# Optimization experiments

Measured on AMD Instinct MI355X. Metric: run time of the kernel, lower is better.

Reference implementation:

```python
import jax, jax.numpy as jnp
import numpy as np

EMBED_DIM = 768
N_HEADS = 12
SEQ_LEN = 577
MAX_REL = 2


def _relative_position_indices(seq_len: int, max_rel: int) -> jnp.ndarray:
    """Static [S, S] int index map into the relative bias table."""
    n_patches = seq_len - 1
    n_per_dim = int(np.sqrt(n_patches))
    n_entries = (2 * max_rel - 1) ** 2
    cls_cls, cls_patch, patch_cls = n_entries, n_entries + 1, n_entries + 2
    idx = np.arange(seq_len)
    qy, qx = (idx - 1) // n_per_dim, (idx - 1) % n_per_dim
    ry = np.clip(qy[:, None] - qy[None, :], -max_rel + 1, max_rel - 1)
    rx = np.clip(qx[:, None] - qx[None, :], -max_rel + 1, max_rel - 1)
    patch_idx = (ry + max_rel - 1) * (2 * max_rel - 1) + (rx + max_rel - 1)
    is_cls = idx == 0
    out = np.where(is_cls[None, :], patch_cls, patch_idx)
    out = np.where(is_cls[:, None], cls_patch, out)
    out = np.where(is_cls[:, None] & is_cls[None, :], cls_cls, out)
    return jnp.asarray(out, dtype=jnp.int32)


def setup_inputs() -> dict:
    key = jax.random.key(0)
    ks = jax.random.split(key, 6)
    e = EMBED_DIM
    scale = 1.0 / np.sqrt(e)
    return {
        "x": jax.random.normal(ks[0], (32, SEQ_LEN, e), dtype=jnp.float32),
        "Wq": jax.random.normal(ks[1], (e, e), dtype=jnp.float32) * scale,
        "Wk": jax.random.normal(ks[2], (e, e), dtype=jnp.float32) * scale,
        "Wv": jax.random.normal(ks[3], (e, e), dtype=jnp.float32) * scale,
        "Wo": jax.random.normal(ks[4], (e, e), dtype=jnp.float32) * scale,
        "bo": jnp.zeros((e,), dtype=jnp.float32),
        "bias_table": jax.random.normal(ks[5], (12,), dtype=jnp.float32) * 0.02,
    }


def reference(x, Wq, Wk, Wv, Wo, bo, bias_table):
    b, s, e = x.shape
    h, d = N_HEADS, e // N_HEADS
    rel_idx = _relative_position_indices(s, MAX_REL)  # [S, S] int32 (static)

    q = (x @ Wq).reshape(b, s, h, d).transpose(0, 2, 1, 3)  # [b,h,s,d]
    k = (x @ Wk).reshape(b, s, h, d).transpose(0, 2, 1, 3)
    v = (x @ Wv).reshape(b, s, h, d).transpose(0, 2, 1, 3)

    scores = jnp.einsum('bhqd,bhkd->bhqk', q, k) / jnp.sqrt(jnp.float32(d))
    bias = jnp.take(bias_table, rel_idx, axis=0)  # [S, S]
    attn = jax.nn.softmax(scores + bias[None, None, :, :], axis=-1)

    out = jnp.einsum('bhqk,bhkd->bhqd', attn, v)
    out = out.transpose(0, 2, 1, 3).reshape(b, s, e)
    return out @ Wo + bo
```

## Files before the change

kernel.cpp:

```cpp
#include <hip/hip_runtime.h>

typedef unsigned short u16;
typedef short short8 __attribute__((ext_vector_type(8)));
typedef float floatx4 __attribute__((ext_vector_type(4)));

#define MFMA16(a, b, c) __builtin_amdgcn_mfma_f32_16x16x32_bf16((a), (b), (c), 0, 0, 0)

__device__ __forceinline__ u16 f2bf(float f) {
  unsigned u = __builtin_bit_cast(unsigned, f);
  u = (u + 0x7fffu + ((u >> 16) & 1u)) >> 16;
  return (u16)u;
}

__device__ __forceinline__ float exp2hw(float x) {
  float r; asm("v_exp_f32 %0, %1" : "=v"(r) : "v"(x)); return r;
}

__device__ __forceinline__ unsigned cvtpk_bf16(float lo, float hi) {
  unsigned r;
  asm("v_cvt_pk_bf16_f32 %0, %1, %2" : "=v"(r) : "v"(lo), "v"(hi));
  return r;
}

__device__ __forceinline__ float bflo(unsigned u) {
  return __builtin_bit_cast(float, u << 16);
}
__device__ __forceinline__ float bfhi(unsigned u) {
  return __builtin_bit_cast(float, u & 0xffff0000u);
}

__device__ __forceinline__ void gload16(const void* g, void* l) {
  typedef __attribute__((address_space(1))) const void GV;
  typedef __attribute__((address_space(3))) void LV;
  __builtin_amdgcn_global_load_lds((GV*)g, (LV*)l, 16, 0, 0);
}


__global__ void cvt_x_kernel(const float* __restrict__ x, u16* __restrict__ xb, int n4) {
  int i = blockIdx.x * 256 + threadIdx.x;
  if (i >= n4) return;
  float4 v = ((const float4*)x)[i];
  ushort4 r; r.x = f2bf(v.x); r.y = f2bf(v.y); r.z = f2bf(v.z); r.w = f2bf(v.w);
  ((ushort4*)xb)[i] = r;
}

__global__ void cvt_wT_kernel(const float* __restrict__ in, u16* __restrict__ out) {
  __shared__ float tile[64][65];
  const int k0 = blockIdx.x * 64, n0 = blockIdx.y * 64;
  const int t = threadIdx.x;
  const int tr = t >> 6, tc = t & 63;
#pragma unroll
  for (int i = 0; i < 16; ++i) {
    int row = i * 4 + tr;
    tile[row][tc] = in[(size_t)(k0 + row) * 768 + n0 + tc];
  }
  __syncthreads();
#pragma unroll
  for (int i = 0; i < 16; ++i) {
    int row = i * 4 + tr;
    out[(size_t)(n0 + row) * 768 + k0 + tc] = f2bf(tile[tc][row]);
  }
}

__global__ void bias_kernel(const float* __restrict__ table, u16* __restrict__ bp) {
  int idx = blockIdx.x * 256 + threadIdx.x;
  if (idx >= 577 * 76) return;
  int q = idx / 76, kb = idx - q * 76;
  u16 o8[8];
#pragma unroll
  for (int j = 0; j < 8; ++j) {
    int k = kb * 8 + j;
    float v = 0.f;
    if (k <= 576) {
      int id;
      if (q == 0 && k == 0) id = 9;
      else if (q == 0) id = 10;
      else if (k == 0) id = 11;
      else {
        int qy = (q - 1) / 24, qx = (q - 1) % 24;
        int ky = (k - 1) / 24, kx = (k - 1) % 24;
        int ry = qy - ky; ry = ry < -1 ? -1 : (ry > 1 ? 1 : ry);
        int rx = qx - kx; rx = rx < -1 ? -1 : (rx > 1 ? 1 : rx);
        id = (ry + 1) * 3 + (rx + 1);
      }
      v = table[id] * 1.4426950408889634f;
    }
    o8[j] = f2bf(v);
  }
  *(uint4*)(bp + ((size_t)kb * 577 + q) * 8) = *(const uint4*)o8;
}

__global__ void zero_vpad(u16* __restrict__ vT) {
  int i = blockIdx.x * 256 + threadIdx.x;
  if (i >= 384 * 64 * 31) return;
  int row = i / 31, c = i - (i / 31) * 31;
  vT[(size_t)row * 608 + 577 + c] = 0;
}


template <int MODE>
__global__ __launch_bounds__(256) void gemm_kernel(
    const u16* __restrict__ A, const u16* __restrict__ BT,
    const int M, const int NBN,
    float* __restrict__ outF, const float* __restrict__ bvec,
    u16* __restrict__ qarr, u16* __restrict__ karr, u16* __restrict__ vTa) {
  constexpr int K = 768;
  __shared__ __align__(16) u16 smem[17408];
  u16* As = smem;
  u16* Bs = smem + 8192;
  u16* Cs = smem;

  const int bid = blockIdx.x;
  const int nb = bid % NBN, mb = bid / NBN;
  const int tid = threadIdx.x;
  const int w = tid >> 6, l = tid & 63;
  const int wr = w >> 1, wc = w & 1;
  const int l15 = l & 15, l4 = l >> 4;
  const int m0 = mb * 128, n0 = nb * 128;

  floatx4 acc[4][4];
#pragma unroll
  for (int i = 0; i < 4; ++i)
#pragma unroll
    for (int j = 0; j < 4; ++j) acc[i][j] = 0.f;

  const int trow = tid >> 2;
  const int tk = (tid & 3) * 8;

  auto stage = [&](int buf, int kt) {
    const int k0 = kt * 32;
#pragma unroll
    for (int i = 0; i < 2; ++i) {
      int row = i * 64 + trow;
      int ar = m0 + row; if (ar >= M) ar = M - 1;
      gload16(A + (size_t)ar * K + k0 + tk, &As[buf * 4096 + row * 32 + tk]);
      int br = n0 + row;
      gload16(BT + (size_t)br * K + k0 + tk, &Bs[buf * 4096 + row * 32 + tk]);
    }
  };

  stage(0, 0);
  __syncthreads();
  int cur = 0;
  for (int kt = 0; kt < 24; ++kt) {
    if (kt + 1 < 24) stage(cur ^ 1, kt + 1);
    short8 af[4], bf[4];
#pragma unroll
    for (int mi = 0; mi < 4; ++mi)
      af[mi] = *(const short8*)&As[cur * 4096 + (wr * 64 + mi * 16 + l15) * 32 + l4 * 8];
#pragma unroll
    for (int ni = 0; ni < 4; ++ni)
      bf[ni] = *(const short8*)&Bs[cur * 4096 + (wc * 64 + ni * 16 + l15) * 32 + l4 * 8];
#pragma unroll
    for (int mi = 0; mi < 4; ++mi)
#pragma unroll
      for (int ni = 0; ni < 4; ++ni)
        acc[mi][ni] = MFMA16(af[mi], bf[ni], acc[mi][ni]);
    __syncthreads();
    cur ^= 1;
  }

  if constexpr (MODE == 0) {
    const int proj = nb / 6;
    const int h0 = (nb - proj * 6) * 2;
    const float qs = (proj == 0) ? 0.18033688011112042f : 1.0f;
#pragma unroll
    for (int mi = 0; mi < 4; ++mi)
#pragma unroll
      for (int i = 0; i < 4; ++i) {
        const int rloc = wr * 64 + mi * 16 + l4 * 4 + i;
#pragma unroll
        for (int ni = 0; ni < 4; ++ni) {
          const int cloc = wc * 64 + ni * 16 + l15;
          Cs[rloc * 136 + cloc] = f2bf(acc[mi][ni][i] * qs);
        }
      }
    __syncthreads();

    if (proj < 2) {
      u16* dst = (proj == 0) ? qarr : karr;
      const int r = tid >> 1, half = tid & 1;
      const int mrow = m0 + r;
      if (mrow < M) {
        const int bq = mrow / 577, sq = mrow - bq * 577;
        u16* base = dst + ((size_t)(bq * 12 + h0 + half) * 577 + sq) * 64;
        const u16* src = Cs + r * 136 + half * 64;
#pragma unroll
        for (int j = 0; j < 8; ++j)
          *(uint4*)(base + j * 8) = *(const uint4*)(src + j * 8);
      }
    } else {
      const int rr = tid & 127, chalf = tid >> 7;
      const int mrow = m0 + rr;
      if (mrow < M) {
        const int bq = mrow / 577, sq = mrow - bq * 577;
        u16* vbase = vTa + ((size_t)(bq * 12 + h0 + chalf) * 64) * 608 + sq;
        const u16* src = Cs + rr * 136 + chalf * 64;
#pragma unroll
        for (int dc = 0; dc < 8; ++dc) {
          const short8 vv = *(const short8*)(src + dc * 8);
#pragma unroll
          for (int jj = 0; jj < 8; ++jj)
            vbase[(size_t)(dc * 8 + jj) * 608] = (u16)vv[jj];
        }
      }
    }
  } else {
#pragma unroll
    for (int mi = 0; mi < 4; ++mi) {
#pragma unroll
      for (int i = 0; i < 4; ++i) {
        const int mrow = m0 + wr * 64 + mi * 16 + l4 * 4 + i;
        if (mrow >= M) continue;
#pragma unroll
        for (int ni = 0; ni < 4; ++ni) {
          const int ncol = n0 + wc * 64 + ni * 16 + l15;
          outF[(size_t)mrow * 768 + ncol] = acc[mi][ni][i] + bvec[ncol];
        }
      }
    }
  }
}


__global__ __launch_bounds__(256, 3) void attn_kernel(
    const u16* __restrict__ qg, const u16* __restrict__ kg,
    const u16* __restrict__ vT, const u16* __restrict__ bp,
    u16* __restrict__ xa) {
  const int bid = (blockIdx.x & 7) * 240 + (blockIdx.x >> 3);
  const int bh = bid / 5, qblk = bid - bh * 5;
  const int tid = threadIdx.x;
  const int w = tid >> 6, l = tid & 63;
  const int l15 = l & 15, l4 = l >> 4;
  const int qbase = qblk * 128 + w * 32;

  const u16* qh = qg + (size_t)bh * 577 * 64;
  const u16* kh = kg + (size_t)bh * 577 * 64;
  const u16* vh = vT + (size_t)bh * 64 * 608;

  __shared__ u16 Ks[2][32 * 64];
  __shared__ u16 Vs[2][32 * 64];

  const int e_ = l >> 3;
  const int s_ = l & 7;
  const int Rk = w * 8 + e_;
  const int kbK = s_ ^ ((4 * w + (e_ & 3)) & 7);
  const int dpV = w * 8 + e_;
  const int dV = 2 * dpV + (s_ >> 2);
  const int kvV = ((s_ & 3) ^ (e_ & 3)) * 8;

  const int sig = ((l15 >> 2) << 3) + (l15 & 3);
  const int sg = l15 & 7;
  const int offA0 = sig * 64 + ((l4 ^ sg)) * 8;
  const int offA1 = sig * 64 + (((l4 | 4) ^ sg)) * 8;
  const int offA2 = offA0 + 256;
  const int offA3 = offA1 + 256;
  const int dpr = l15 >> 1;
  const int offV = dpr * 64 + (((l15 & 1) << 2) + (l4 ^ (dpr & 3))) * 8;

  short8 qf[2][2];
  int bq[2];
#pragma unroll
  for (int g = 0; g < 2; ++g) {
    int qr = qbase + g * 16 + l15; if (qr > 576) qr = 576;
    bq[g] = qr;
    qf[g][0] = *(const short8*)(qh + qr * 64 + l4 * 8);
    qf[g][1] = *(const short8*)(qh + qr * 64 + 32 + l4 * 8);
  }

  floatx4 o[2][4];
  float m[2] = {-1e30f, -1e30f}, lsum[2] = {0.f, 0.f};
#pragma unroll
  for (int g = 0; g < 2; ++g)
#pragma unroll
    for (int d = 0; d < 4; ++d) o[g][d] = 0.f;

  {
    int kr = Rk; if (kr > 576) kr = 576;
    gload16(kh + (size_t)kr * 64 + kbK * 8, &Ks[0][w * 512 + l * 8]);
    gload16(vh + (size_t)dV * 608 + kvV, &Vs[0][w * 512 + l * 8]);
  }
  uint4 bc0 = *(const uint4*)(bp + ((size_t)l4 * 577 + bq[0]) * 8);
  uint4 bc1 = *(const uint4*)(bp + ((size_t)l4 * 577 + bq[1]) * 8);
  __syncthreads();

  for (int t = 0; t < 19; ++t) {
    const int cur = t & 1;
    const int kvb = t * 32;

    uint4 nb0 = bc0, nb1 = bc1;
    if (t < 18) {
      const int nkvb = kvb + 32;
      int kr = nkvb + Rk; if (kr > 576) kr = 576;
      gload16(kh + (size_t)kr * 64 + kbK * 8, &Ks[cur ^ 1][w * 512 + l * 8]);
      gload16(vh + (size_t)dV * 608 + nkvb + kvV, &Vs[cur ^ 1][w * 512 + l * 8]);
      const int nkb = (t + 1) * 4 + l4;
      nb0 = *(const uint4*)(bp + ((size_t)nkb * 577 + bq[0]) * 8);
      nb1 = *(const uint4*)(bp + ((size_t)nkb * 577 + bq[1]) * 8);
    }

    const u16* kb_ = &Ks[cur][0];
    const short8 A0 = *(const short8*)(kb_ + offA0);
    const short8 A1 = *(const short8*)(kb_ + offA1);
    const short8 A2 = *(const short8*)(kb_ + offA2);
    const short8 A3 = *(const short8*)(kb_ + offA3);
    const u16* vb_ = &Vs[cur][0];
    const short8 vf0 = *(const short8*)(vb_ + offV);
    const short8 vf1 = *(const short8*)(vb_ + offV + 512);
    const short8 vf2 = *(const short8*)(vb_ + offV + 1024);
    const short8 vf3 = *(const short8*)(vb_ + offV + 1536);

    float v0[8], v1[8];
    {
      floatx4 s0 = 0.f, s1 = 0.f, s2 = 0.f, s3 = 0.f;
      __builtin_amdgcn_s_setprio(1);
      s0 = MFMA16(A0, qf[0][0], s0);
      s0 = MFMA16(A1, qf[0][1], s0);
      s1 = MFMA16(A2, qf[0][0], s1);
      s1 = MFMA16(A3, qf[0][1], s1);
      s2 = MFMA16(A0, qf[1][0], s2);
      s2 = MFMA16(A1, qf[1][1], s2);
      s3 = MFMA16(A2, qf[1][0], s3);
      s3 = MFMA16(A3, qf[1][1], s3);
      __builtin_amdgcn_s_setprio(0);
      v0[0] = s0[0] + bflo(bc0.x); v0[1] = s0[1] + bfhi(bc0.x);
      v0[2] = s0[2] + bflo(bc0.y); v0[3] = s0[3] + bfhi(bc0.y);
      v0[4] = s1[0] + bflo(bc0.z); v0[5] = s1[1] + bfhi(bc0.z);
      v0[6] = s1[2] + bflo(bc0.w); v0[7] = s1[3] + bfhi(bc0.w);
      v1[0] = s2[0] + bflo(bc1.x); v1[1] = s2[1] + bfhi(bc1.x);
      v1[2] = s2[2] + bflo(bc1.y); v1[3] = s2[3] + bfhi(bc1.y);
      v1[4] = s3[0] + bflo(bc1.z); v1[5] = s3[1] + bfhi(bc1.z);
      v1[6] = s3[2] + bflo(bc1.w); v1[7] = s3[3] + bfhi(bc1.w);
    }

    if (t == 18) {
      const int kg0 = kvb + l4 * 8;
#pragma unroll
      for (int j = 0; j < 8; ++j)
        if (kg0 + j > 576) { v0[j] = -1e30f; v1[j] = -1e30f; }
    }

    float vmA = fmaxf(fmaxf(fmaxf(v0[0], v0[1]), fmaxf(v0[2], v0[3])),
                      fmaxf(fmaxf(v0[4], v0[5]), fmaxf(v0[6], v0[7])));
    float vmB = fmaxf(fmaxf(fmaxf(v1[0], v1[1]), fmaxf(v1[2], v1[3])),
                      fmaxf(fmaxf(v1[4], v1[5]), fmaxf(v1[6], v1[7])));
    vmA = fmaxf(vmA, __shfl_xor(vmA, 16)); vmA = fmaxf(vmA, __shfl_xor(vmA, 32));
    vmB = fmaxf(vmB, __shfl_xor(vmB, 16)); vmB = fmaxf(vmB, __shfl_xor(vmB, 32));

    if (__any((vmA > m[0] + 8.f) || (vmB > m[1] + 8.f))) {
      const float mn0 = fmaxf(m[0], vmA), mn1 = fmaxf(m[1], vmB);
      const float sc0 = exp2hw(m[0] - mn0), sc1 = exp2hw(m[1] - mn1);
      lsum[0] *= sc0; lsum[1] *= sc1;
#pragma unroll
      for (int d = 0; d < 4; ++d) { o[0][d] *= sc0; o[1][d] *= sc1; }
      m[0] = mn0; m[1] = mn1;
    }

    float e0[8], e1[8];
    float rs0 = 0.f, rs1 = 0.f;
#pragma unroll
    for (int j = 0; j < 8; ++j) { e0[j] = exp2hw(v0[j] - m[0]); rs0 += e0[j]; }
#pragma unroll
    for (int j = 0; j < 8; ++j) { e1[j] = exp2hw(v1[j] - m[1]); rs1 += e1[j]; }
    rs0 += __shfl_xor(rs0, 16); rs0 += __shfl_xor(rs0, 32);
    rs1 += __shfl_xor(rs1, 16); rs1 += __shfl_xor(rs1, 32);
    lsum[0] += rs0; lsum[1] += rs1;

    union PU { unsigned u[4]; short8 s; };
    PU p0, p1;
#pragma unroll
    for (int j = 0; j < 4; ++j) {
      p0.u[j] = cvtpk_bf16(e0[2 * j], e0[2 * j + 1]);
      p1.u[j] = cvtpk_bf16(e1[2 * j], e1[2 * j + 1]);
    }

    __builtin_amdgcn_s_setprio(1);
    o[0][0] = MFMA16(vf0, p0.s, o[0][0]);
    o[1][0] = MFMA16(vf0, p1.s, o[1][0]);
    o[0][1] = MFMA16(vf1, p0.s, o[0][1]);
    o[1][1] = MFMA16(vf1, p1.s, o[1][1]);
    o[0][2] = MFMA16(vf2, p0.s, o[0][2]);
    o[1][2] = MFMA16(vf2, p1.s, o[1][2]);
    o[0][3] = MFMA16(vf3, p0.s, o[0][3]);
    o[1][3] = MFMA16(vf3, p1.s, o[1][3]);
    __builtin_amdgcn_s_setprio(0);

    bc0 = nb0; bc1 = nb1;
    __syncthreads();
  }

  const int b = bh / 12, h = bh - (bh / 12) * 12;
#pragma unroll
  for (int g = 0; g < 2; ++g) {
    const int gq = qbase + g * 16 + l15;
    if (gq < 577) {
      const float inv = 1.f / lsum[g];
      u16* op = xa + ((size_t)(b * 577 + gq)) * 768 + h * 64 + l4 * 4;
#pragma unroll
      for (int d = 0; d < 4; ++d) {
        unsigned w0 = cvtpk_bf16(o[g][d][0] * inv, o[g][d][1] * inv);
        unsigned w1 = cvtpk_bf16(o[g][d][2] * inv, o[g][d][3] * inv);
        *(unsigned*)(op + d * 16) = w0;
        *(unsigned*)(op + d * 16 + 2) = w1;
      }
    }
  }
}


extern "C" void kernel_launch(void* const* d_in, const int* in_sizes, int n_in,
                              void* d_out, int out_size, void* d_ws, size_t ws_size,
                              hipStream_t stream) {
  const float* x  = (const float*)d_in[0];
  const float* Wq = (const float*)d_in[1];
  const float* Wk = (const float*)d_in[2];
  const float* Wv = (const float*)d_in[3];
  const float* Wo = (const float*)d_in[4];
  const float* bo = (const float*)d_in[5];
  const float* bt = (const float*)d_in[6];
  float* out = (float*)d_out;

  char* ws = (char*)d_ws;
  size_t off = 0;
  auto alloc = [&](size_t bytes) {
    void* p = ws + off;
    off += (bytes + 255) & ~(size_t)255;
    return p;
  };
  u16* xb   = (u16*)alloc((size_t)18464 * 768 * 2);
  u16* WT   = (u16*)alloc((size_t)2304 * 768 * 2);
  u16* WoT  = (u16*)alloc((size_t)768 * 768 * 2);
  u16* qa   = (u16*)alloc((size_t)384 * 577 * 64 * 2);
  u16* ka   = (u16*)alloc((size_t)384 * 577 * 64 * 2);
  u16* vT   = (u16*)alloc((size_t)384 * 64 * 608 * 2);
  u16* biasPk = (u16*)alloc((size_t)76 * 577 * 8 * 2);
  (void)ws_size; (void)in_sizes; (void)n_in; (void)out_size;

  zero_vpad<<<(384 * 64 * 31 + 255) / 256, 256, 0, stream>>>(vT);
  cvt_x_kernel<<<(18464 * 768 / 4 + 255) / 256, 256, 0, stream>>>(x, xb, 18464 * 768 / 4);
  dim3 tg(12, 12);
  cvt_wT_kernel<<<tg, 256, 0, stream>>>(Wq, WT);
  cvt_wT_kernel<<<tg, 256, 0, stream>>>(Wk, WT + (size_t)768 * 768);
  cvt_wT_kernel<<<tg, 256, 0, stream>>>(Wv, WT + (size_t)2 * 768 * 768);
  cvt_wT_kernel<<<tg, 256, 0, stream>>>(Wo, WoT);
  bias_kernel<<<(577 * 76 + 255) / 256, 256, 0, stream>>>(bt, biasPk);

  gemm_kernel<0><<<145 * 18, 256, 0, stream>>>(xb, WT, 18464, 18,
                                               nullptr, nullptr, qa, ka, vT);
  attn_kernel<<<1920, 256, 0, stream>>>(qa, ka, vT, biasPk, xb);
  gemm_kernel<1><<<145 * 6, 256, 0, stream>>>(xb, WoT, 18464, 6,
                                              out, bo, nullptr, nullptr, nullptr);
}
```

Before: 258.9 us.

## Use 64-key attention tiles, peel last key into init, remap GEMM blocks per XCD

The attention kernel now processes 64 keys per iteration over 9 tiles instead of 32 keys over 19. The 577th key is handled up front: its score seeds the running max with lsum=1 and its V row seeds the accumulator. This removes the masked tail iteration and the zero_vpad kernel, at the cost of a small extra bias576 kernel. K/V shared-memory tiles double in size with a new XOR swizzle, and the occupancy hint drops from 3 to 2 blocks per CU. The GEMM block index is remapped so consecutive tiles land on the same XCD, for better L2 locality.

```diff
diff --git a/kernel.cpp b/kernel.cpp
--- a/kernel.cpp
+++ b/kernel.cpp
@@ -10,6 +10,10 @@
   unsigned u = __builtin_bit_cast(unsigned, f);
   u = (u + 0x7fffu + ((u >> 16) & 1u)) >> 16;
   return (u16)u;
+}
+
+__device__ __forceinline__ float bf2f(u16 u) {
+  return __builtin_bit_cast(float, ((unsigned)u) << 16);
 }
 
 __device__ __forceinline__ float exp2hw(float x) {
@@ -90,11 +94,18 @@
   *(uint4*)(bp + ((size_t)kb * 577 + q) * 8) = *(const uint4*)o8;
 }
 
-__global__ void zero_vpad(u16* __restrict__ vT) {
-  int i = blockIdx.x * 256 + threadIdx.x;
-  if (i >= 384 * 64 * 31) return;
-  int row = i / 31, c = i - (i / 31) * 31;
-  vT[(size_t)row * 608 + 577 + c] = 0;
+__global__ void bias576_kernel(const float* __restrict__ table, float* __restrict__ b576) {
+  int q = blockIdx.x * 256 + threadIdx.x;
+  if (q >= 577) return;
+  int id;
+  if (q == 0) id = 10;
+  else {
+    int qy = (q - 1) / 24, qx = (q - 1) % 24;
+    int ry = qy - 23; ry = ry < -1 ? -1 : (ry > 1 ? 1 : ry);
+    int rx = qx - 23; rx = rx < -1 ? -1 : (rx > 1 ? 1 : rx);
+    id = (ry + 1) * 3 + (rx + 1);
+  }
+  b576[q] = table[id] * 1.4426950408889634f;
 }
 
 
@@ -110,7 +121,11 @@
   u16* Bs = smem + 8192;
   u16* Cs = smem;
 
-  const int bid = blockIdx.x;
+  const int nwg = gridDim.x;
+  const int q8 = nwg >> 3, r8 = nwg & 7;
+  const int xcd = blockIdx.x & 7, jj = blockIdx.x >> 3;
+  const int bid = ((xcd < r8) ? xcd * (q8 + 1) : r8 * (q8 + 1) + (xcd - r8) * q8) + jj;
+
   const int nb = bid % NBN, mb = bid / NBN;
   const int tid = threadIdx.x;
   const int w = tid >> 6, l = tid & 63;
@@ -200,8 +215,8 @@
         for (int dc = 0; dc < 8; ++dc) {
           const short8 vv = *(const short8*)(src + dc * 8);
 #pragma unroll
-          for (int jj = 0; jj < 8; ++jj)
-            vbase[(size_t)(dc * 8 + jj) * 608] = (u16)vv[jj];
+          for (int jjx = 0; jjx < 8; ++jjx)
+            vbase[(size_t)(dc * 8 + jjx) * 608] = (u16)vv[jjx];
         }
       }
     }
@@ -223,10 +238,10 @@
 }
 
 
-__global__ __launch_bounds__(256, 3) void attn_kernel(
+__global__ __launch_bounds__(256, 2) void attn_kernel(
     const u16* __restrict__ qg, const u16* __restrict__ kg,
     const u16* __restrict__ vT, const u16* __restrict__ bp,
-    u16* __restrict__ xa) {
+    const float* __restrict__ b576, u16* __restrict__ xa) {
   const int bid = (blockIdx.x & 7) * 240 + (blockIdx.x >> 3);
   const int bh = bid / 5, qblk = bid - bh * 5;
   const int tid = threadIdx.x;
@@ -238,25 +253,33 @@
   const u16* kh = kg + (size_t)bh * 577 * 64;
   const u16* vh = vT + (size_t)bh * 64 * 608;
 
-  __shared__ u16 Ks[2][32 * 64];
-  __shared__ u16 Vs[2][32 * 64];
-
-  const int e_ = l >> 3;
-  const int s_ = l & 7;
-  const int Rk = w * 8 + e_;
-  const int kbK = s_ ^ ((4 * w + (e_ & 3)) & 7);
-  const int dpV = w * 8 + e_;
-  const int dV = 2 * dpV + (s_ >> 2);
-  const int kvV = ((s_ & 3) ^ (e_ & 3)) * 8;
+  __shared__ u16 Ks[2][64 * 64];
+  __shared__ u16 Vs[2][64 * 64];
+
+  const int sr = tid >> 3;
+  const int sb = tid & 7;
+  const int ss = ((sr & 7) ^ ((2 * (sr >> 3)) & 7)) & 7;
+  const int scol = (sb ^ ss) * 8;
 
   const int sig = ((l15 >> 2) << 3) + (l15 & 3);
-  const int sg = l15 & 7;
-  const int offA0 = sig * 64 + ((l4 ^ sg)) * 8;
-  const int offA1 = sig * 64 + (((l4 | 4) ^ sg)) * 8;
-  const int offA2 = offA0 + 256;
-  const int offA3 = offA1 + 256;
-  const int dpr = l15 >> 1;
-  const int offV = dpr * 64 + (((l15 & 1) << 2) + (l4 ^ (dpr & 3))) * 8;
+  const int s0_ = ((l15 & 3) ^ ((2 * (l15 >> 2)) & 7)) & 7;
+  const int s4_ = s0_ ^ 4;
+  const int oK00 = sig * 64 + ((l4 ^ s0_) << 3);
+  const int oK01 = sig * 64 + (((l4 + 4) ^ s0_) << 3);
+  const int oK10 = (sig + 4) * 64 + ((l4 ^ s4_) << 3);
+  const int oK11 = (sig + 4) * 64 + (((l4 + 4) ^ s4_) << 3);
+  const int oK20 = oK00 + 32 * 64;
+  const int oK21 = oK01 + 32 * 64;
+  const int oK30 = oK10 + 32 * 64;
+  const int oK31 = oK11 + 32 * 64;
+  int oV[4][2];
+#pragma unroll
+  for (int df = 0; df < 4; ++df) {
+    const int r = df * 16 + l15;
+    const int sv = ((r & 7) ^ ((2 * (r >> 3)) & 7)) & 7;
+    oV[df][0] = r * 64 + ((l4 ^ sv) << 3);
+    oV[df][1] = r * 64 + (((l4 + 4) ^ sv) << 3);
+  }
 
   short8 qf[2][2];
   int bq[2];
@@ -268,124 +291,149 @@
     qf[g][1] = *(const short8*)(qh + qr * 64 + 32 + l4 * 8);
   }
 
+  float m[2], lsum[2] = {1.f, 1.f};
+  {
+    const u16* kp = kh + 576 * 64 + l4 * 8;
+    const short8 kA = *(const short8*)(kp);
+    const short8 kB = *(const short8*)(kp + 32);
+#pragma unroll
+    for (int g = 0; g < 2; ++g) {
+      float acc = 0.f;
+#pragma unroll
+      for (int j = 0; j < 8; ++j)
+        acc += bf2f((u16)qf[g][0][j]) * bf2f((u16)kA[j]) +
+               bf2f((u16)qf[g][1][j]) * bf2f((u16)kB[j]);
+      acc += __shfl_xor(acc, 16);
+      acc += __shfl_xor(acc, 32);
+      m[g] = acc + b576[bq[g]];
+    }
+  }
   floatx4 o[2][4];
-  float m[2] = {-1e30f, -1e30f}, lsum[2] = {0.f, 0.f};
-#pragma unroll
-  for (int g = 0; g < 2; ++g)
-#pragma unroll
-    for (int d = 0; d < 4; ++d) o[g][d] = 0.f;
-
-  {
-    int kr = Rk; if (kr > 576) kr = 576;
-    gload16(kh + (size_t)kr * 64 + kbK * 8, &Ks[0][w * 512 + l * 8]);
-    gload16(vh + (size_t)dV * 608 + kvV, &Vs[0][w * 512 + l * 8]);
-  }
-  uint4 bc0 = *(const uint4*)(bp + ((size_t)l4 * 577 + bq[0]) * 8);
-  uint4 bc1 = *(const uint4*)(bp + ((size_t)l4 * 577 + bq[1]) * 8);
+#pragma unroll
+  for (int df = 0; df < 4; ++df)
+#pragma unroll
+    for (int i = 0; i < 4; ++i) {
+      const float v5 = bf2f(vh[(size_t)(df * 16 + l4 * 4 + i) * 608 + 576]);
+      o[0][df][i] = v5; o[1][df][i] = v5;
+    }
+
+  gload16(kh + (size_t)sr * 64 + scol, &Ks[0][sr * 64 + sb * 8]);
+  gload16(kh + (size_t)(sr + 32) * 64 + scol, &Ks[0][(sr + 32) * 64 + sb * 8]);
+  gload16(vh + (size_t)sr * 608 + scol, &Vs[0][sr * 64 + sb * 8]);
+  gload16(vh + (size_t)(sr + 32) * 608 + scol, &Vs[0][(sr + 32) * 64 + sb * 8]);
   __syncthreads();
 
-  for (int t = 0; t < 19; ++t) {
+  for (int t = 0; t < 9; ++t) {
     const int cur = t & 1;
-    const int kvb = t * 32;
-
-    uint4 nb0 = bc0, nb1 = bc1;
-    if (t < 18) {
-      const int nkvb = kvb + 32;
-      int kr = nkvb + Rk; if (kr > 576) kr = 576;
-      gload16(kh + (size_t)kr * 64 + kbK * 8, &Ks[cur ^ 1][w * 512 + l * 8]);
-      gload16(vh + (size_t)dV * 608 + nkvb + kvV, &Vs[cur ^ 1][w * 512 + l * 8]);
-      const int nkb = (t + 1) * 4 + l4;
-      nb0 = *(const uint4*)(bp + ((size_t)nkb * 577 + bq[0]) * 8);
-      nb1 = *(const uint4*)(bp + ((size_t)nkb * 577 + bq[1]) * 8);
-    }
+    if (t < 8) {
+      const int nk = (t + 1) * 64;
+      gload16(kh + (size_t)(nk + sr) * 64 + scol, &Ks[cur ^ 1][sr * 64 + sb * 8]);
+      gload16(kh + (size_t)(nk + sr + 32) * 64 + scol, &Ks[cur ^ 1][(sr + 32) * 64 + sb * 8]);
+      gload16(vh + (size_t)sr * 608 + nk + scol, &Vs[cur ^ 1][sr * 64 + sb * 8]);
+      gload16(vh + (size_t)(sr + 32) * 608 + nk + scol, &Vs[cur ^ 1][(sr + 32) * 64 + sb * 8]);
+    }
+
+    const int kba = t * 8 + l4;
+    const uint4 ba0 = *(const uint4*)(bp + ((size_t)kba * 577 + bq[0]) * 8);
+    const uint4 bb0 = *(const uint4*)(bp + ((size_t)(kba + 4) * 577 + bq[0]) * 8);
+    const uint4 ba1 = *(const uint4*)(bp + ((size_t)kba * 577 + bq[1]) * 8);
+    const uint4 bb1 = *(const uint4*)(bp + ((size_t)(kba + 4) * 577 + bq[1]) * 8);
 
     const u16* kb_ = &Ks[cur][0];
-    const short8 A0 = *(const short8*)(kb_ + offA0);
-    const short8 A1 = *(const short8*)(kb_ + offA1);
-    const short8 A2 = *(const short8*)(kb_ + offA2);
-    const short8 A3 = *(const short8*)(kb_ + offA3);
-    const u16* vb_ = &Vs[cur][0];
-    const short8 vf0 = *(const short8*)(vb_ + offV);
-    const short8 vf1 = *(const short8*)(vb_ + offV + 512);
-    const short8 vf2 = *(const short8*)(vb_ + offV + 1024);
-    const short8 vf3 = *(const short8*)(vb_ + offV + 1536);
-
-    float v0[8], v1[8];
-    {
-      floatx4 s0 = 0.f, s1 = 0.f, s2 = 0.f, s3 = 0.f;
-      __builtin_amdgcn_s_setprio(1);
-      s0 = MFMA16(A0, qf[0][0], s0);
-      s0 = MFMA16(A1, qf[0][1], s0);
-      s1 = MFMA16(A2, qf[0][0], s1);
-      s1 = MFMA16(A3, qf[0][1], s1);
-      s2 = MFMA16(A0, qf[1][0], s2);
-      s2 = MFMA16(A1, qf[1][1], s2);
-      s3 = MFMA16(A2, qf[1][0], s3);
-      s3 = MFMA16(A3, qf[1][1], s3);
-      __builtin_amdgcn_s_setprio(0);
-      v0[0] = s0[0] + bflo(bc0.x); v0[1] = s0[1] + bfhi(bc0.x);
-      v0[2] = s0[2] + bflo(bc0.y); v0[3] = s0[3] + bfhi(bc0.y);
-      v0[4] = s1[0] + bflo(bc0.z); v0[5] = s1[1] + bfhi(bc0.z);
-      v0[6] = s1[2] + bflo(bc0.w); v0[7] = s1[3] + bfhi(bc0.w);
-      v1[0] = s2[0] + bflo(bc1.x); v1[1] = s2[1] + bfhi(bc1.x);
-      v1[2] = s2[2] + bflo(bc1.y); v1[3] = s2[3] + bfhi(bc1.y);
-      v1[4] = s3[0] + bflo(bc1.z); v1[5] = s3[1] + bfhi(bc1.z);
-      v1[6] = s3[2] + bflo(bc1.w); v1[7] = s3[3] + bfhi(bc1.w);
-    }
-
-    if (t == 18) {
-      const int kg0 = kvb + l4 * 8;
-#pragma unroll
-      for (int j = 0; j < 8; ++j)
-        if (kg0 + j > 576) { v0[j] = -1e30f; v1[j] = -1e30f; }
-    }
-
-    float vmA = fmaxf(fmaxf(fmaxf(v0[0], v0[1]), fmaxf(v0[2], v0[3])),
-                      fmaxf(fmaxf(v0[4], v0[5]), fmaxf(v0[6], v0[7])));
-    float vmB = fmaxf(fmaxf(fmaxf(v1[0], v1[1]), fmaxf(v1[2], v1[3])),
-                      fmaxf(fmaxf(v1[4], v1[5]), fmaxf(v1[6], v1[7])));
-    vmA = fmaxf(vmA, __shfl_xor(vmA, 16)); vmA = fmaxf(vmA, __shfl_xor(vmA, 32));
-    vmB = fmaxf(vmB, __shfl_xor(vmB, 16)); vmB = fmaxf(vmB, __shfl_xor(vmB, 32));
-
-    if (__any((vmA > m[0] + 8.f) || (vmB > m[1] + 8.f))) {
-      const float mn0 = fmaxf(m[0], vmA), mn1 = fmaxf(m[1], vmB);
+    const short8 K00 = *(const short8*)(kb_ + oK00);
+    const short8 K01 = *(const short8*)(kb_ + oK01);
+    const short8 K10 = *(const short8*)(kb_ + oK10);
+    const short8 K11 = *(const short8*)(kb_ + oK11);
+    const short8 K20 = *(const short8*)(kb_ + oK20);
+    const short8 K21 = *(const short8*)(kb_ + oK21);
+    const short8 K30 = *(const short8*)(kb_ + oK30);
+    const short8 K31 = *(const short8*)(kb_ + oK31);
+
+    floatx4 sA0[2], sA1[2], sB0[2], sB1[2];
+    __builtin_amdgcn_s_setprio(1);
+#pragma unroll
+    for (int g = 0; g < 2; ++g) {
+      floatx4 a0 = 0.f, a1 = 0.f, b0 = 0.f, b1 = 0.f;
+      a0 = MFMA16(K00, qf[g][0], a0); a0 = MFMA16(K01, qf[g][1], a0);
+      a1 = MFMA16(K10, qf[g][0], a1); a1 = MFMA16(K11, qf[g][1], a1);
+      b0 = MFMA16(K20, qf[g][0], b0); b0 = MFMA16(K21, qf[g][1], b0);
+      b1 = MFMA16(K30, qf[g][0], b1); b1 = MFMA16(K31, qf[g][1], b1);
+      sA0[g] = a0; sA1[g] = a1; sB0[g] = b0; sB1[g] = b1;
+    }
+    __builtin_amdgcn_s_setprio(0);
+
+    float v_[2][16];
+#pragma unroll
+    for (int g = 0; g < 2; ++g) {
+      const uint4 ba = (g == 0) ? ba0 : ba1;
+      const uint4 bb = (g == 0) ? bb0 : bb1;
+      v_[g][0] = sA0[g][0] + bflo(ba.x);  v_[g][1] = sA0[g][1] + bfhi(ba.x);
+      v_[g][2] = sA0[g][2] + bflo(ba.y);  v_[g][3] = sA0[g][3] + bfhi(ba.y);
+      v_[g][4] = sA1[g][0] + bflo(ba.z);  v_[g][5] = sA1[g][1] + bfhi(ba.z);
+      v_[g][6] = sA1[g][2] + bflo(ba.w);  v_[g][7] = sA1[g][3] + bfhi(ba.w);
+      v_[g][8]  = sB0[g][0] + bflo(bb.x); v_[g][9]  = sB0[g][1] + bfhi(bb.x);
+      v_[g][10] = sB0[g][2] + bflo(bb.y); v_[g][11] = sB0[g][3] + bfhi(bb.y);
+      v_[g][12] = sB1[g][0] + bflo(bb.z); v_[g][13] = sB1[g][1] + bfhi(bb.z);
+      v_[g][14] = sB1[g][2] + bflo(bb.w); v_[g][15] = sB1[g][3] + bfhi(bb.w);
+    }
+
+    float vm[2];
+#pragma unroll
+    for (int g = 0; g < 2; ++g) {
+      float a = v_[g][0];
+#pragma unroll
+      for (int j = 1; j < 16; ++j) a = fmaxf(a, v_[g][j]);
+      a = fmaxf(a, __shfl_xor(a, 16));
+      a = fmaxf(a, __shfl_xor(a, 32));
+      vm[g] = a;
+    }
+
+    if (__any((vm[0] > m[0] + 8.f) || (vm[1] > m[1] + 8.f))) {
+      const float mn0 = fmaxf(m[0], vm[0]), mn1 = fmaxf(m[1], vm[1]);
       const float sc0 = exp2hw(m[0] - mn0), sc1 = exp2hw(m[1] - mn1);
       lsum[0] *= sc0; lsum[1] *= sc1;
 #pragma unroll
-      for (int d = 0; d < 4; ++d) { o[0][d] *= sc0; o[1][d] *= sc1; }
+      for (int df = 0; df < 4; ++df) { o[0][df] *= sc0; o[1][df] *= sc1; }
       m[0] = mn0; m[1] = mn1;
     }
 
-    float e0[8], e1[8];
-    float rs0 = 0.f, rs1 = 0.f;
-#pragma unroll
-    for (int j = 0; j < 8; ++j) { e0[j] = exp2hw(v0[j] - m[0]); rs0 += e0[j]; }
-#pragma unroll
-    for (int j = 0; j < 8; ++j) { e1[j] = exp2hw(v1[j] - m[1]); rs1 += e1[j]; }
-    rs0 += __shfl_xor(rs0, 16); rs0 += __shfl_xor(rs0, 32);
-    rs1 += __shfl_xor(rs1, 16); rs1 += __shfl_xor(rs1, 32);
-    lsum[0] += rs0; lsum[1] += rs1;
-
     union PU { unsigned u[4]; short8 s; };
-    PU p0, p1;
-#pragma unroll
-    for (int j = 0; j < 4; ++j) {
-      p0.u[j] = cvtpk_bf16(e0[2 * j], e0[2 * j + 1]);
-      p1.u[j] = cvtpk_bf16(e1[2 * j], e1[2 * j + 1]);
-    }
+    PU pA[2], pB[2];
+#pragma unroll
+    for (int g = 0; g < 2; ++g) {
+      float rs = 0.f;
+#pragma unroll
+      for (int j = 0; j < 16; ++j) { v_[g][j] = exp2hw(v_[g][j] - m[g]); rs += v_[g][j]; }
+      rs += __shfl_xor(rs, 16);
+      rs += __shfl_xor(rs, 32);
+      lsum[g] += rs;
+#pragma unroll
+      for (int j = 0; j < 4; ++j) {
+        pA[g].u[j] = cvtpk_bf16(v_[g][2 * j], v_[g][2 * j + 1]);
+        pB[g].u[j] = cvtpk_bf16(v_[g][8 + 2 * j], v_[g][8 + 2 * j + 1]);
+      }
+    }
+
+    const u16* vb_ = &Vs[cur][0];
+    const short8 vA0 = *(const short8*)(vb_ + oV[0][0]);
+    const short8 vB0 = *(const short8*)(vb_ + oV[0][1]);
+    const short8 vA1 = *(const short8*)(vb_ + oV[1][0]);
+    const short8 vB1 = *(const short8*)(vb_ + oV[1][1]);
+    const short8 vA2 = *(const short8*)(vb_ + oV[2][0]);
+    const short8 vB2 = *(const short8*)(vb_ + oV[2][1]);
+    const short8 vA3 = *(const short8*)(vb_ + oV[3][0]);
+    const short8 vB3 = *(const short8*)(vb_ + oV[3][1]);
 
     __builtin_amdgcn_s_setprio(1);
-    o[0][0] = MFMA16(vf0, p0.s, o[0][0]);
-    o[1][0] = MFMA16(vf0, p1.s, o[1][0]);
-    o[0][1] = MFMA16(vf1, p0.s, o[0][1]);
-    o[1][1] = MFMA16(vf1, p1.s, o[1][1]);
-    o[0][2] = MFMA16(vf2, p0.s, o[0][2]);
-    o[1][2] = MFMA16(vf2, p1.s, o[1][2]);
-    o[0][3] = MFMA16(vf3, p0.s, o[0][3]);
-    o[1][3] = MFMA16(vf3, p1.s, o[1][3]);
+#pragma unroll
+    for (int g = 0; g < 2; ++g) {
+      o[g][0] = MFMA16(vA0, pA[g].s, o[g][0]); o[g][0] = MFMA16(vB0, pB[g].s, o[g][0]);
+      o[g][1] = MFMA16(vA1, pA[g].s, o[g][1]); o[g][1] = MFMA16(vB1, pB[g].s, o[g][1]);
+      o[g][2] = MFMA16(vA2, pA[g].s, o[g][2]); o[g][2] = MFMA16(vB2, pB[g].s, o[g][2]);
+      o[g][3] = MFMA16(vA3, pA[g].s, o[g][3]); o[g][3] = MFMA16(vB3, pB[g].s, o[g][3]);
+    }
     __builtin_amdgcn_s_setprio(0);
 
-    bc0 = nb0; bc1 = nb1;
     __syncthreads();
   }
 
@@ -434,9 +482,9 @@
   u16* ka   = (u16*)alloc((size_t)384 * 577 * 64 * 2);
   u16* vT   = (u16*)alloc((size_t)384 * 64 * 608 * 2);
   u16* biasPk = (u16*)alloc((size_t)76 * 577 * 8 * 2);
+  float* b576 = (float*)alloc((size_t)577 * 4);
   (void)ws_size; (void)in_sizes; (void)n_in; (void)out_size;
 
-  zero_vpad<<<(384 * 64 * 31 + 255) / 256, 256, 0, stream>>>(vT);
   cvt_x_kernel<<<(18464 * 768 / 4 + 255) / 256, 256, 0, stream>>>(x, xb, 18464 * 768 / 4);
   dim3 tg(12, 12);
   cvt_wT_kernel<<<tg, 256, 0, stream>>>(Wq, WT);
@@ -444,10 +492,11 @@
   cvt_wT_kernel<<<tg, 256, 0, stream>>>(Wv, WT + (size_t)2 * 768 * 768);
   cvt_wT_kernel<<<tg, 256, 0, stream>>>(Wo, WoT);
   bias_kernel<<<(577 * 76 + 255) / 256, 256, 0, stream>>>(bt, biasPk);
+  bias576_kernel<<<3, 256, 0, stream>>>(bt, b576);
 
   gemm_kernel<0><<<145 * 18, 256, 0, stream>>>(xb, WT, 18464, 18,
                                                nullptr, nullptr, qa, ka, vT);
-  attn_kernel<<<1920, 256, 0, stream>>>(qa, ka, vT, biasPk, xb);
+  attn_kernel<<<1920, 256, 0, stream>>>(qa, ka, vT, biasPk, b576, xb);
   gemm_kernel<1><<<145 * 6, 256, 0, stream>>>(xb, WoT, 18464, 6,
                                               out, bo, nullptr, nullptr, nullptr);
 }
```

New measurement: 247.6 us. -4.4%, faster.
